# Performance work log

Hardware: AMD Instinct MI355X
Metric: run time of the kernel (lower is better)

## Reference

```python
import jax, jax.numpy as jnp
import numpy as np

EPS = 1e-12

def _l2n(x):
    # torch F.normalize(p=2, dim=0): x / max(||x||_2, eps)
    return x / jnp.maximum(jnp.linalg.norm(x), EPS)

def _gru_cell(x, h, Wi, Wh, bi, bh):
    # torch GRU cell math; Wi:(3H,Din), Wh:(3H,H)
    gi = Wi @ x + bi
    gh = Wh @ h + bh
    i_r, i_z, i_n = jnp.split(gi, 3)
    h_r, h_z, h_n = jnp.split(gh, 3)
    r = jax.nn.sigmoid(i_r + h_r)
    z = jax.nn.sigmoid(i_z + h_z)
    n = jnp.tanh(i_n + r * h_n)
    return (1.0 - z) * n + z * h

def setup_inputs() -> dict:
    key = jax.random.key(0)
    ks = jax.random.split(key, 20)
    m, n, T = 10, 10, 100
    H1, H2, HID = 1600, 400, 2000
    D_in, D_out = 2 * m + n, m * n
    f32 = jnp.float32
    inp = {
        'y': jax.random.normal(ks[0], (n, T), f32),
        'm1x_0': jax.random.normal(ks[1], (m,), f32),
        'F': jax.random.normal(ks[2], (m, m), f32) * 0.1,
        'Hm': jax.random.normal(ks[3], (n, m), f32) * 0.1,
        'h0': jax.random.normal(ks[4], (2, HID), f32),
        'W1': jax.random.normal(ks[5], (H1, D_in), f32) * 0.05,
        'b1': jax.random.normal(ks[6], (H1,), f32) * 0.05,
        'Wi0': jax.random.normal(ks[7], (3 * HID, H1), f32) * 0.02,
        'Wh0': jax.random.normal(ks[8], (3 * HID, HID), f32) * 0.02,
        'bi0': jax.random.normal(ks[9], (3 * HID,), f32) * 0.02,
        'bh0': jax.random.normal(ks[10], (3 * HID,), f32) * 0.02,
        'Wi1': jax.random.normal(ks[11], (3 * HID, HID), f32) * 0.02,
        'Wh1': jax.random.normal(ks[12], (3 * HID, HID), f32) * 0.02,
        'bi1': jax.random.normal(ks[13], (3 * HID,), f32) * 0.02,
        'bh1': jax.random.normal(ks[14], (3 * HID,), f32) * 0.02,
        'W2': jax.random.normal(ks[15], (H2, HID), f32) * 0.02,
        'b2': jax.random.normal(ks[16], (H2,), f32) * 0.02,
        'W3': jax.random.normal(ks[17], (D_out, H2), f32) * 0.01,
        'b3': jax.random.normal(ks[18], (D_out,), f32) * 0.01,
    }
    return inp

def reference(y, m1x_0, F, Hm, h0, W1, b1, Wi0, Wh0, bi0, bh0,
              Wi1, Wh1, bi1, bh1, W2, b2, W3, b3):
    n, T = y.shape
    m = m1x_0.shape[0]
    # first step uses obs_process_0 = h(f(m1x_0)) as y_previous surrogate
    y_prev0 = Hm @ (F @ m1x_0)
    carry0 = (m1x_0, jnp.zeros_like(m1x_0), m1x_0, y_prev0, h0[0], h0[1])

    def step(carry, yt):
        post, prev_post, prev_prior, y_prev, h1, h2 = carry
        prior = F @ post              # step_prior
        m1y = Hm @ prior
        f1 = _l2n(yt - y_prev)        # innovation diff feature
        f3 = _l2n(post - prev_post)   # posterior update feature
        f4 = _l2n(post - prev_prior)  # residual feature
        kin = jnp.concatenate([f1, f3, f4])  # (2m+n,)
        a = jax.nn.relu(W1 @ kin + b1)
        h1n = _gru_cell(a, h1, Wi0, Wh0, bi0, bh0)
        h2n = _gru_cell(h1n, h2, Wi1, Wh1, bi1, bh1)
        g = jax.nn.relu(W2 @ h2n + b2)
        KG = (W3 @ g + b3).reshape(m, n)
        dy = yt - m1y
        new_post = prior + KG @ dy
        return (new_post, post, prior, yt, h1n, h2n), new_post

    _, xs = jax.lax.scan(step, carry0, y.T)  # xs: (T, m)
    return xs.T  # (m, T)
```

## Files before the change

### kernel.cpp

```cpp
#include <hip/hip_runtime.h>
#include <math.h>

#define NB 256
#define NT 1024
#define NW 16
#define TT 100
#define MM 10
#define NN 10
#define HID 2000
#define H1 1600
#define H2 400
#define G3 6000
#define KP 2048
#define RPB 24

#define SCOPE_AGENT __HIP_MEMORY_SCOPE_AGENT

typedef _Float16 h2v __attribute__((ext_vector_type(2)));

__device__ __forceinline__ float sigf(float x) { return 1.f / (1.f + __expf(-x)); }
__device__ __forceinline__ float tanhfast(float x) { return 2.f / (1.f + __expf(-2.f * x)) - 1.f; }

__device__ __forceinline__ float ld_coh(const float* p) {
  return __hip_atomic_load(p, __ATOMIC_RELAXED, SCOPE_AGENT);
}
__device__ __forceinline__ void st_coh(float* p, float v) {
  __hip_atomic_store(p, v, __ATOMIC_RELAXED, SCOPE_AGENT);
}
__device__ __forceinline__ float2 ld_coh2(const float* p) {
  unsigned long long v = __hip_atomic_load((const unsigned long long*)p,
                                           __ATOMIC_RELAXED, SCOPE_AGENT);
  union { unsigned long long u; float2 f; } c; c.u = v; return c.f;
}
__device__ __forceinline__ void stage_coh(const float* __restrict__ src,
                                          float* __restrict__ dst, int n, int tid) {
  const int n2 = n >> 1;
  for (int j = tid; j < n2; j += NT) {
    float2 v = ld_coh2(src + 2 * j);
    dst[2 * j]     = v.x;
    dst[2 * j + 1] = v.y;
  }
}

__device__ __forceinline__ void gridbar(unsigned* flags, unsigned* release,
                                        unsigned ep, int tid, int blk) {
  __syncthreads();
  if (tid == 0)
    __hip_atomic_store(flags + blk * 16, ep, __ATOMIC_RELAXED, SCOPE_AGENT);
  if (blk == 0) {
    if (tid < NB) {
      while (__hip_atomic_load(flags + tid * 16, __ATOMIC_RELAXED, SCOPE_AGENT) < ep)
        __builtin_amdgcn_s_sleep(1);
    }
    __syncthreads();
    if (tid == 0)
      __hip_atomic_store(release, ep, __ATOMIC_RELAXED, SCOPE_AGENT);
  } else {
    if (tid == 0) {
      while (__hip_atomic_load(release, __ATOMIC_RELAXED, SCOPE_AGENT) < ep)
        __builtin_amdgcn_s_sleep(1);
    }
  }
  __syncthreads();
}

__device__ __forceinline__ void set_flag(unsigned* f, unsigned v, int tid) {
  __syncthreads();
  if (tid == 0) __hip_atomic_store(f, v, __ATOMIC_RELAXED, SCOPE_AGENT);
}
__device__ __forceinline__ void wait_flag(const unsigned* f, unsigned v, int tid) {
  if (tid == 0) {
    while (__hip_atomic_load(f, __ATOMIC_RELAXED, SCOPE_AGENT) < v)
      __builtin_amdgcn_s_sleep(1);
  }
  __syncthreads();
}

template<int K>
__device__ __forceinline__ float rowdotT(const float* __restrict__ row,
                                         const float* __restrict__ x, int ln) {
  constexpr int NFULL = K / 256;
  constexpr int REM   = K - NFULL * 256;
  const int base = ln * 4;
  float4 w[NFULL + (REM ? 1 : 0)];
  #pragma unroll
  for (int i = 0; i < NFULL; ++i)
    w[i] = *reinterpret_cast<const float4*>(row + base + i * 256);
  bool tail = false;
  if constexpr (REM != 0) {
    tail = (base + NFULL * 256 + 3 < K);
    if (tail) w[NFULL] = *reinterpret_cast<const float4*>(row + base + NFULL * 256);
  }
  float acc = 0.f;
  #pragma unroll
  for (int i = 0; i < NFULL; ++i) {
    const float4 xv = *reinterpret_cast<const float4*>(x + base + i * 256);
    acc = fmaf(w[i].x, xv.x, acc);
    acc = fmaf(w[i].y, xv.y, acc);
    acc = fmaf(w[i].z, xv.z, acc);
    acc = fmaf(w[i].w, xv.w, acc);
  }
  if constexpr (REM != 0) {
    if (tail) {
      const float4 xv = *reinterpret_cast<const float4*>(x + base + NFULL * 256);
      acc = fmaf(w[NFULL].x, xv.x, acc);
      acc = fmaf(w[NFULL].y, xv.y, acc);
      acc = fmaf(w[NFULL].z, xv.z, acc);
      acc = fmaf(w[NFULL].w, xv.w, acc);
    }
  }
  #pragma unroll
  for (int off = 32; off; off >>= 1) acc += __shfl_xor(acc, off, 64);
  return acc;
}

__device__ __forceinline__ void sweep24(const _Float16* __restrict__ W,
                                        const float* __restrict__ bias,
                                        int row0, int nrows,
                                        const _Float16* __restrict__ xh,
                                        float* __restrict__ outw,
                                        bool relu,
                                        int wv, int ln, int tid, float* red,
                                        float* __restrict__ gloc)
{
  const _Float16* wp = W + (size_t)row0 * KP + wv * 3072 + ln * 8;
  uint4 w[6];
  #pragma unroll
  for (int c = 0; c < 6; ++c)
    w[c] = *reinterpret_cast<const uint4*>(wp + c * 512);
  float a0 = 0.f, a1 = 0.f;
  const int first = (3 * wv) >> 1;
  #pragma unroll
  for (int c = 0; c < 6; ++c) {
    const int flat = wv * 3072 + c * 512;
    const int sel  = (flat >> 11) - first;
    const int col  = (flat & (KP - 1)) + ln * 8;
    const uint4 xv = *reinterpret_cast<const uint4*>(xh + col);
    union { uint4 u; h2v h[4]; } wu, xu;
    wu.u = w[c]; xu.u = xv;
    float acc = sel ? a1 : a0;
    #pragma unroll
    for (int q = 0; q < 4; ++q)
      acc = __builtin_amdgcn_fdot2(wu.h[q], xu.h[q], acc, false);
    if (sel) a1 = acc; else a0 = acc;
  }
  #pragma unroll
  for (int off = 32; off; off >>= 1) {
    a0 += __shfl_xor(a0, off, 64);
    a1 += __shfl_xor(a1, off, 64);
  }
  __syncthreads();
  if (ln == 0) { red[wv * 2] = a0; red[wv * 2 + 1] = a1; }
  __syncthreads();
  if (tid < nrows) {
    const int k = tid / 3, m = tid % 3;
    float v = (m == 0) ? red[4 * k]
            : (m == 1) ? red[4 * k + 1] + red[4 * k + 2]
                       : red[4 * k + 3];
    v += bias[row0 + tid];
    if (relu) v = fmaxf(v, 0.f);
    if (gloc) gloc[tid] = v;
    st_coh(outw + row0 + tid, v);
  }
}

__global__ __launch_bounds__(256)
void convh(const float* __restrict__ src, _Float16* __restrict__ dst,
           int rows, int K, int padrows) {
  const size_t total = (size_t)padrows * KP;
  for (size_t i = (size_t)blockIdx.x * blockDim.x + threadIdx.x; i < total;
       i += (size_t)gridDim.x * blockDim.x) {
    const int r = (int)(i >> 11), c = (int)(i & (KP - 1));
    float v = (r < rows && c < K) ? src[(size_t)r * K + c] : 0.f;
    dst[i] = (_Float16)v;
  }
}
__global__ __launch_bounds__(256)
void convw1(const float* __restrict__ src, _Float16* __restrict__ dst) {
  const int i = blockIdx.x * 256 + threadIdx.x;
  const int r = i >> 5, c = i & 31;
  float v = (r < H1 && c < 30) ? src[r * 30 + c] : 0.f;
  dst[i] = (_Float16)v;
}

__global__ __launch_bounds__(NT)
void knet_f16(const float* __restrict__ y, const float* __restrict__ m1x0,
              const float* __restrict__ F, const float* __restrict__ Hm,
              const float* __restrict__ h0,
              const float* __restrict__ W1, const float* __restrict__ b1,
              const float* __restrict__ Wi0, const float* __restrict__ Wh0,
              const float* __restrict__ bi0, const float* __restrict__ bh0,
              const float* __restrict__ Wi1, const float* __restrict__ Wh1,
              const float* __restrict__ bi1, const float* __restrict__ bh1,
              const float* __restrict__ W2, const float* __restrict__ b2,
              const float* __restrict__ W3, const float* __restrict__ b3,
              float* __restrict__ out, float* __restrict__ ws)
{
  const int blk = blockIdx.x, tid = threadIdx.x;
  const int wv = tid >> 6, ln = tid & 63;

  float* a_ws     = ws;
  float* gi0_ws   = ws + 1600;
  float* gh0_ws   = ws + 7600;
  float* gi1_ws   = ws + 13600;
  float* gh1b     = ws + 19600;
  float* g_ws     = ws + 31600;
  float* vpart_ws = ws + 32000;
  unsigned* flags   = (unsigned*)(ws + 33728);
  unsigned* release = flags + 256 * 16;
  unsigned* vflag   = release + 16;
  unsigned* aflag   = vflag + 17 * 16;

  const _Float16* whbase = (const _Float16*)((const char*)ws + 152576);
  const _Float16* Wi0h = whbase;
  const _Float16* Wh0h = whbase + (size_t)G3 * KP;
  const _Float16* Wi1h = whbase + (size_t)2 * G3 * KP;
  const _Float16* Wh1h = whbase + (size_t)3 * G3 * KP;
  const _Float16* W2h  = whbase + (size_t)4 * G3 * KP;
  const _Float16* W1h  = whbase + (size_t)4 * G3 * KP + (size_t)408 * KP;

  __shared__ __align__(16) _Float16 ah[KP];
  __shared__ __align__(16) _Float16 h1h[KP];
  __shared__ __align__(16) _Float16 h2h[KP];
  __shared__ __align__(16) float h1l[HID];
  __shared__ __align__(16) float h2l[HID];
  __shared__ __align__(16) float xs[1728];
  __shared__ __align__(16) _Float16 kin_h[32];
  __shared__ float red[32];
  __shared__ float gloc_s[RPB];
  __shared__ float post_s[MM], prevpost_s[MM], prevprior_s[MM], prior_s[MM];
  __shared__ float dy_s[NN], yprev_s[NN], tmp_s[MM];
  __shared__ float d1_s[NN], d3_s[MM], d4_s[MM];
  __shared__ float kin_s[32], nrm_s[3];
  __shared__ float v_s[MM * NN], np_s[MM];

  for (int j = tid; j < HID; j += NT) {
    float v1 = h0[j], v2 = h0[HID + j];
    h1l[j] = v1; h2l[j] = v2;
    h1h[j] = (_Float16)v1; h2h[j] = (_Float16)v2;
  }
  for (int j = HID + tid; j < KP; j += NT) { h1h[j] = (_Float16)0.f; h2h[j] = (_Float16)0.f; }
  for (int j = H1 + tid; j < KP; j += NT) ah[j] = (_Float16)0.f;
  __syncthreads();

  unsigned ep = 0;

  for (int t = 0; t < TT; ++t) {
    float* gh1w = gh1b + (t & 1) * G3;
    float* gh1r = gh1b + ((t + 1) & 1) * G3;

    if (blk == NB - 1) {
      if (t > 0) {
        if (tid < 17) {
          while (__hip_atomic_load(vflag + tid * 16, __ATOMIC_RELAXED, SCOPE_AGENT) < (unsigned)t)
            __builtin_amdgcn_s_sleep(1);
        }
        __syncthreads();
        stage_coh(vpart_ws, xs, 1700, tid);
        __syncthreads();
        if (tid < MM * NN) {
          float s = b3[tid];
          #pragma unroll
          for (int k = 0; k < 17; ++k) s += xs[k * 100 + tid];
          v_s[tid] = s;
        }
        __syncthreads();
        if (tid < MM) {
          float np = prior_s[tid];
          #pragma unroll
          for (int j = 0; j < NN; ++j) np = fmaf(v_s[tid * NN + j], dy_s[j], np);
          out[tid * TT + (t - 1)] = np;
          np_s[tid] = np;
        }
        __syncthreads();
        if (tid < MM) {
          prevpost_s[tid]  = post_s[tid];
          prevprior_s[tid] = prior_s[tid];
          post_s[tid]      = np_s[tid];
        }
        __syncthreads();
      } else {
        if (tid < MM) {
          post_s[tid]      = m1x0[tid];
          prevpost_s[tid]  = 0.f;
          prevprior_s[tid] = m1x0[tid];
          float tv = 0.f;
          for (int j = 0; j < MM; ++j) tv = fmaf(F[tid * MM + j], m1x0[j], tv);
          tmp_s[tid] = tv;
        }
        __syncthreads();
        if (tid < NN) {
          float yp = 0.f;
          for (int j = 0; j < MM; ++j) yp = fmaf(Hm[tid * MM + j], tmp_s[j], yp);
          yprev_s[tid] = yp;
        }
        __syncthreads();
      }
      if (tid < MM) {
        float pr = 0.f;
        for (int j = 0; j < MM; ++j) pr = fmaf(F[tid * MM + j], post_s[j], pr);
        prior_s[tid] = pr;
      }
      __syncthreads();
      if (tid < NN) {
        float my = 0.f;
        for (int j = 0; j < MM; ++j) my = fmaf(Hm[tid * MM + j], prior_s[j], my);
        float yt = y[tid * TT + t];
        dy_s[tid] = yt - my;
        d1_s[tid] = yt - ((t == 0) ? yprev_s[tid] : y[tid * TT + (t - 1)]);
        d3_s[tid] = post_s[tid] - prevpost_s[tid];
        d4_s[tid] = post_s[tid] - prevprior_s[tid];
      }
      __syncthreads();
      if (tid == 0) {
        float n1 = 0.f, n3 = 0.f, n4 = 0.f;
        for (int j = 0; j < NN; ++j) n1 += d1_s[j] * d1_s[j];
        for (int j = 0; j < MM; ++j) { n3 += d3_s[j] * d3_s[j]; n4 += d4_s[j] * d4_s[j]; }
        nrm_s[0] = fmaxf(sqrtf(n1), 1e-12f);
        nrm_s[1] = fmaxf(sqrtf(n3), 1e-12f);
        nrm_s[2] = fmaxf(sqrtf(n4), 1e-12f);
      }
      __syncthreads();
      if (tid < NN) kin_s[tid] = d1_s[tid] / nrm_s[0];
      if (tid < MM) {
        kin_s[NN + tid]      = d3_s[tid] / nrm_s[1];
        kin_s[NN + MM + tid] = d4_s[tid] / nrm_s[2];
      }
      __syncthreads();
      if (tid < 32) kin_h[tid] = (_Float16)((tid < 30) ? kin_s[tid] : 0.f);
      __syncthreads();
      if (tid < 800) {
        const _Float16* wp = W1h + (size_t)tid * 64;
        uint4 q[8];
        #pragma unroll
        for (int c = 0; c < 8; ++c)
          q[c] = *reinterpret_cast<const uint4*>(wp + c * 8);
        const uint4* kq = reinterpret_cast<const uint4*>(kin_h);
        union { uint4 u; h2v h[4]; } kk[4], qq;
        #pragma unroll
        for (int c = 0; c < 4; ++c) kk[c].u = kq[c];
        const int r0 = 2 * tid;
        float s0 = b1[r0], s1 = b1[r0 + 1];
        #pragma unroll
        for (int c = 0; c < 4; ++c) {
          qq.u = q[c];
          #pragma unroll
          for (int p = 0; p < 4; ++p)
            s0 = __builtin_amdgcn_fdot2(qq.h[p], kk[c].h[p], s0, false);
        }
        #pragma unroll
        for (int c = 0; c < 4; ++c) {
          qq.u = q[c + 4];
          #pragma unroll
          for (int p = 0; p < 4; ++p)
            s1 = __builtin_amdgcn_fdot2(qq.h[p], kk[c].h[p], s1, false);
        }
        st_coh(a_ws + r0,     fmaxf(s0, 0.f));
        st_coh(a_ws + r0 + 1, fmaxf(s1, 0.f));
      }
      set_flag(aflag, (unsigned)(t + 1), tid);
    } else {
      if (blk >= 17) {
        if (blk <= 249) {
          sweep24(Wh0h, bh0, RPB * (blk - 17), RPB, h1h, gh0_ws, false, wv, ln, tid, red, nullptr);
        } else {
          #pragma unroll
          for (int i = 0; i < 4; ++i) {
            const int task = 233 + (blk - 250) + 5 * i;
            if (task < 250)
              sweep24(Wh0h, bh0, RPB * task, RPB, h1h, gh0_ws, false, wv, ln, tid, red, nullptr);
          }
        }
      }
      if (t > 0) {
        for (int j = tid; j < HID / 2; j += NT) {
          float2 ir = ld_coh2(gi1_ws + 2 * j),            hr = ld_coh2(gh1r + 2 * j);
          float2 iz = ld_coh2(gi1_ws + HID + 2 * j),      hz = ld_coh2(gh1r + HID + 2 * j);
          float2 in_ = ld_coh2(gi1_ws + 2 * HID + 2 * j), hn = ld_coh2(gh1r + 2 * HID + 2 * j);
          float r0 = sigf(ir.x + hr.x), r1 = sigf(ir.y + hr.y);
          float z0 = sigf(iz.x + hz.x), z1 = sigf(iz.y + hz.y);
          float n0 = tanhfast(in_.x + r0 * hn.x), n1 = tanhfast(in_.y + r1 * hn.y);
          float o0 = (1.f - z0) * n0 + z0 * h2l[2 * j];
          float o1 = (1.f - z1) * n1 + z1 * h2l[2 * j + 1];
          h2l[2 * j] = o0; h2l[2 * j + 1] = o1;
          h2h[2 * j] = (_Float16)o0; h2h[2 * j + 1] = (_Float16)o1;
        }
        __syncthreads();
        if (blk < 17) {
          const int row0 = RPB * blk;
          const int nr = (H2 - row0 < RPB) ? (H2 - row0) : RPB;
          sweep24(W2h, b2, row0, nr, h2h, g_ws, true, wv, ln, tid, red, gloc_s);
          __syncthreads();
          if (tid < MM * NN) {
            float s = 0.f;
            const float* w3c = W3 + (size_t)tid * H2 + row0;
            for (int j = 0; j < nr; ++j) s = fmaf(w3c[j], gloc_s[j], s);
            st_coh(vpart_ws + blk * 100 + tid, s);
          }
          set_flag(vflag + blk * 16, (unsigned)t, tid);
        }
      }
      if (blk <= 249)
        sweep24(Wh1h, bh1, RPB * blk, RPB, h2h, gh1w, false, wv, ln, tid, red, nullptr);
      if (blk <= 249) {
        wait_flag(aflag, (unsigned)(t + 1), tid);
        const int n2 = H1 >> 1;
        for (int j = tid; j < n2; j += NT) {
          float2 v = ld_coh2(a_ws + 2 * j);
          ah[2 * j]     = (_Float16)v.x;
          ah[2 * j + 1] = (_Float16)v.y;
        }
        __syncthreads();
        sweep24(Wi0h, bi0, RPB * blk, RPB, ah, gi0_ws, false, wv, ln, tid, red, nullptr);
      }
    }
    ++ep; gridbar(flags, release, ep, tid, blk);

    if (blk != NB - 1) {
      for (int j = tid; j < HID / 2; j += NT) {
        float2 ir = ld_coh2(gi0_ws + 2 * j),            hr = ld_coh2(gh0_ws + 2 * j);
        float2 iz = ld_coh2(gi0_ws + HID + 2 * j),      hz = ld_coh2(gh0_ws + HID + 2 * j);
        float2 in_ = ld_coh2(gi0_ws + 2 * HID + 2 * j), hn = ld_coh2(gh0_ws + 2 * HID + 2 * j);
        float r0 = sigf(ir.x + hr.x), r1 = sigf(ir.y + hr.y);
        float z0 = sigf(iz.x + hz.x), z1 = sigf(iz.y + hz.y);
        float n0 = tanhfast(in_.x + r0 * hn.x), n1 = tanhfast(in_.y + r1 * hn.y);
        float o0 = (1.f - z0) * n0 + z0 * h1l[2 * j];
        float o1 = (1.f - z1) * n1 + z1 * h1l[2 * j + 1];
        h1l[2 * j] = o0; h1l[2 * j + 1] = o1;
        h1h[2 * j] = (_Float16)o0; h1h[2 * j + 1] = (_Float16)o1;
      }
      __syncthreads();
      if (blk <= 249)
        sweep24(Wi1h, bi1, RPB * blk, RPB, h1h, gi1_ws, false, wv, ln, tid, red, nullptr);
    }
    ++ep; gridbar(flags, release, ep, tid, blk);
  }

  if (blk < 17) {
    float* gh1r = gh1b + ((TT + 1) & 1) * G3;
    for (int j = tid; j < HID / 2; j += NT) {
      float2 ir = ld_coh2(gi1_ws + 2 * j),            hr = ld_coh2(gh1r + 2 * j);
      float2 iz = ld_coh2(gi1_ws + HID + 2 * j),      hz = ld_coh2(gh1r + HID + 2 * j);
      float2 in_ = ld_coh2(gi1_ws + 2 * HID + 2 * j), hn = ld_coh2(gh1r + 2 * HID + 2 * j);
      float r0 = sigf(ir.x + hr.x), r1 = sigf(ir.y + hr.y);
      float z0 = sigf(iz.x + hz.x), z1 = sigf(iz.y + hz.y);
      float n0 = tanhfast(in_.x + r0 * hn.x), n1 = tanhfast(in_.y + r1 * hn.y);
      float o0 = (1.f - z0) * n0 + z0 * h2l[2 * j];
      float o1 = (1.f - z1) * n1 + z1 * h2l[2 * j + 1];
      h2h[2 * j] = (_Float16)o0; h2h[2 * j + 1] = (_Float16)o1;
    }
    __syncthreads();
    const int row0 = RPB * blk;
    const int nr = (H2 - row0 < RPB) ? (H2 - row0) : RPB;
    sweep24(W2h, b2, row0, nr, h2h, g_ws, true, wv, ln, tid, red, gloc_s);
    __syncthreads();
    if (tid < MM * NN) {
      float s = 0.f;
      const float* w3c = W3 + (size_t)tid * H2 + row0;
      for (int j = 0; j < nr; ++j) s = fmaf(w3c[j], gloc_s[j], s);
      st_coh(vpart_ws + blk * 100 + tid, s);
    }
    set_flag(vflag + blk * 16, (unsigned)TT, tid);
  }
  if (blk == NB - 1) {
    if (tid < 17) {
      while (__hip_atomic_load(vflag + tid * 16, __ATOMIC_RELAXED, SCOPE_AGENT) < (unsigned)TT)
        __builtin_amdgcn_s_sleep(1);
    }
    __syncthreads();
    stage_coh(vpart_ws, xs, 1700, tid);
    __syncthreads();
    if (tid < MM * NN) {
      float s = b3[tid];
      #pragma unroll
      for (int k = 0; k < 17; ++k) s += xs[k * 100 + tid];
      v_s[tid] = s;
    }
    __syncthreads();
    if (tid < MM) {
      float np = prior_s[tid];
      #pragma unroll
      for (int j = 0; j < NN; ++j) np = fmaf(v_s[tid * NN + j], dy_s[j], np);
      out[tid * TT + (TT - 1)] = np;
    }
  }
}

__global__ __launch_bounds__(NT)
void knet_f32(const float* __restrict__ y, const float* __restrict__ m1x0,
              const float* __restrict__ F, const float* __restrict__ Hm,
              const float* __restrict__ h0,
              const float* __restrict__ W1, const float* __restrict__ b1,
              const float* __restrict__ Wi0, const float* __restrict__ Wh0,
              const float* __restrict__ bi0, const float* __restrict__ bh0,
              const float* __restrict__ Wi1, const float* __restrict__ Wh1,
              const float* __restrict__ bi1, const float* __restrict__ bh1,
              const float* __restrict__ W2, const float* __restrict__ b2,
              const float* __restrict__ W3, const float* __restrict__ b3,
              float* __restrict__ out, float* __restrict__ ws)
{
  const int blk = blockIdx.x, tid = threadIdx.x;
  const int wv = tid >> 6, ln = tid & 63;

  float* a_ws   = ws;
  float* gi0_ws = ws + 1600;
  float* gh0_ws = ws + 7600;
  float* gi1_ws = ws + 13600;
  float* gh1_ws = ws + 19600;
  float* g_ws   = ws + 25600;
  unsigned* flags   = (unsigned*)(ws + 26624);
  unsigned* release = flags + NB * 16;

  __shared__ __align__(16) float xs[1664];
  __shared__ __align__(16) float h1l[HID];
  __shared__ __align__(16) float h2l[HID];
  __shared__ float post_s[MM], prevpost_s[MM], prevprior_s[MM], prior_s[MM];
  __shared__ float dy_s[NN], yprev_s[NN], tmp_s[MM];
  __shared__ float d1_s[NN], d3_s[MM], d4_s[MM];
  __shared__ float kin_s[32], nrm_s[3];
  __shared__ float v_s[MM * NN], np_s[MM];

  for (int j = tid; j < HID; j += NT) { h1l[j] = h0[j]; h2l[j] = h0[HID + j]; }
  __syncthreads();

  unsigned ep = 0;

  for (int t = 0; t < TT; ++t) {
    if (blk == NB - 1) {
      if (t > 0) {
        stage_coh(g_ws, xs, H2, tid);
        __syncthreads();
        for (int r = wv; r < MM * NN; r += NW) {
          float acc = rowdotT<H2>(W3 + (size_t)r * H2, xs, ln);
          if (ln == 0) v_s[r] = acc + b3[r];
        }
        __syncthreads();
        if (tid < MM) {
          float np = prior_s[tid];
          #pragma unroll
          for (int j = 0; j < NN; ++j) np = fmaf(v_s[tid * NN + j], dy_s[j], np);
          out[tid * TT + (t - 1)] = np;
          np_s[tid] = np;
        }
        __syncthreads();
        if (tid < MM) {
          prevpost_s[tid]  = post_s[tid];
          prevprior_s[tid] = prior_s[tid];
          post_s[tid]      = np_s[tid];
        }
        __syncthreads();
      } else {
        if (tid < MM) {
          post_s[tid]      = m1x0[tid];
          prevpost_s[tid]  = 0.f;
          prevprior_s[tid] = m1x0[tid];
          float tv = 0.f;
          for (int j = 0; j < MM; ++j) tv = fmaf(F[tid * MM + j], m1x0[j], tv);
          tmp_s[tid] = tv;
        }
        __syncthreads();
        if (tid < NN) {
          float yp = 0.f;
          for (int j = 0; j < MM; ++j) yp = fmaf(Hm[tid * MM + j], tmp_s[j], yp);
          yprev_s[tid] = yp;
        }
        __syncthreads();
      }
      if (tid < MM) {
        float pr = 0.f;
        for (int j = 0; j < MM; ++j) pr = fmaf(F[tid * MM + j], post_s[j], pr);
        prior_s[tid] = pr;
      }
      __syncthreads();
      if (tid < NN) {
        float my = 0.f;
        for (int j = 0; j < MM; ++j) my = fmaf(Hm[tid * MM + j], prior_s[j], my);
        float yt = y[tid * TT + t];
        dy_s[tid] = yt - my;
        d1_s[tid] = yt - ((t == 0) ? yprev_s[tid] : y[tid * TT + (t - 1)]);
        d3_s[tid] = post_s[tid] - prevpost_s[tid];
        d4_s[tid] = post_s[tid] - prevprior_s[tid];
      }
      __syncthreads();
      if (tid == 0) {
        float n1 = 0.f, n3 = 0.f, n4 = 0.f;
        for (int j = 0; j < NN; ++j) n1 += d1_s[j] * d1_s[j];
        for (int j = 0; j < MM; ++j) { n3 += d3_s[j] * d3_s[j]; n4 += d4_s[j] * d4_s[j]; }
        nrm_s[0] = fmaxf(sqrtf(n1), 1e-12f);
        nrm_s[1] = fmaxf(sqrtf(n3), 1e-12f);
        nrm_s[2] = fmaxf(sqrtf(n4), 1e-12f);
      }
      __syncthreads();
      if (tid < NN) kin_s[tid] = d1_s[tid] / nrm_s[0];
      if (tid < MM) {
        kin_s[NN + tid]      = d3_s[tid] / nrm_s[1];
        kin_s[NN + MM + tid] = d4_s[tid] / nrm_s[2];
      }
      __syncthreads();
      for (int r = tid; r < H1; r += NT) {
        float acc = b1[r];
        const float* row = W1 + (size_t)r * 30;
        #pragma unroll
        for (int k = 0; k < 30; ++k) acc = fmaf(row[k], kin_s[k], acc);
        st_coh(a_ws + r, fmaxf(acc, 0.f));
      }
    } else {
      const int gw = blk * NW + wv;
      for (int r = gw; r < G3; r += (NB - 1) * NW) {
        float acc = rowdotT<HID>(Wh1 + (size_t)r * HID, h2l, ln);
        if (ln == 0) st_coh(gh1_ws + r, acc + bh1[r]);
      }
      if (t == 0) {
        for (int r = gw; r < G3; r += (NB - 1) * NW) {
          float acc = rowdotT<HID>(Wh0 + (size_t)r * HID, h1l, ln);
          if (ln == 0) st_coh(gh0_ws + r, acc + bh0[r]);
        }
      }
    }
    ++ep; gridbar(flags, release, ep, tid, blk);

    stage_coh(a_ws, xs, H1, tid);
    __syncthreads();
    {
      const int gw = blk * NW + wv;
      for (int r = gw; r < G3; r += NB * NW) {
        float acc = rowdotT<H1>(Wi0 + (size_t)r * H1, xs, ln);
        if (ln == 0) st_coh(gi0_ws + r, acc + bi0[r]);
      }
    }
    ++ep; gridbar(flags, release, ep, tid, blk);

    {
      for (int j = tid; j < HID / 2; j += NT) {
        float2 ir = ld_coh2(gi0_ws + 2 * j),            hr = ld_coh2(gh0_ws + 2 * j);
        float2 iz = ld_coh2(gi0_ws + HID + 2 * j),      hz = ld_coh2(gh0_ws + HID + 2 * j);
        float2 in_ = ld_coh2(gi0_ws + 2 * HID + 2 * j), hn = ld_coh2(gh0_ws + 2 * HID + 2 * j);
        float r0 = sigf(ir.x + hr.x), r1 = sigf(ir.y + hr.y);
        float z0 = sigf(iz.x + hz.x), z1 = sigf(iz.y + hz.y);
        float n0 = tanhfast(in_.x + r0 * hn.x), n1 = tanhfast(in_.y + r1 * hn.y);
        h1l[2 * j]     = (1.f - z0) * n0 + z0 * h1l[2 * j];
        h1l[2 * j + 1] = (1.f - z1) * n1 + z1 * h1l[2 * j + 1];
      }
      __syncthreads();
      const int gw = blk * NW + wv;
      for (int r = gw; r < G3; r += NB * NW) {
        float acc = rowdotT<HID>(Wi1 + (size_t)r * HID, h1l, ln);
        if (ln == 0) st_coh(gi1_ws + r, acc + bi1[r]);
      }
    }
    ++ep; gridbar(flags, release, ep, tid, blk);

    {
      for (int j = tid; j < HID / 2; j += NT) {
        float2 ir = ld_coh2(gi1_ws + 2 * j),            hr = ld_coh2(gh1_ws + 2 * j);
        float2 iz = ld_coh2(gi1_ws + HID + 2 * j),      hz = ld_coh2(gh1_ws + HID + 2 * j);
        float2 in_ = ld_coh2(gi1_ws + 2 * HID + 2 * j), hn = ld_coh2(gh1_ws + 2 * HID + 2 * j);
        float r0 = sigf(ir.x + hr.x), r1 = sigf(ir.y + hr.y);
        float z0 = sigf(iz.x + hz.x), z1 = sigf(iz.y + hz.y);
        float n0 = tanhfast(in_.x + r0 * hn.x), n1 = tanhfast(in_.y + r1 * hn.y);
        h2l[2 * j]     = (1.f - z0) * n0 + z0 * h2l[2 * j];
        h2l[2 * j + 1] = (1.f - z1) * n1 + z1 * h2l[2 * j + 1];
      }
      __syncthreads();
      const int gw = blk * NW + wv;
      for (int r = gw; r < H2 + G3; r += NB * NW) {
        if (r < H2) {
          float acc = rowdotT<HID>(W2 + (size_t)r * HID, h2l, ln);
          if (ln == 0) st_coh(g_ws + r, fmaxf(acc + b2[r], 0.f));
        } else {
          const int rr = r - H2;
          float acc = rowdotT<HID>(Wh0 + (size_t)rr * HID, h1l, ln);
          if (ln == 0) st_coh(gh0_ws + rr, acc + bh0[rr]);
        }
      }
    }
    ++ep; gridbar(flags, release, ep, tid, blk);
  }

  if (blk == NB - 1) {
    stage_coh(g_ws, xs, H2, tid);
    __syncthreads();
    for (int r = wv; r < MM * NN; r += NW) {
      float acc = rowdotT<H2>(W3 + (size_t)r * H2, xs, ln);
      if (ln == 0) v_s[r] = acc + b3[r];
    }
    __syncthreads();
    if (tid < MM) {
      float np = prior_s[tid];
      #pragma unroll
      for (int j = 0; j < NN; ++j) np = fmaf(v_s[tid * NN + j], dy_s[j], np);
      out[tid * TT + (TT - 1)] = np;
    }
  }
}

extern "C" void kernel_launch(void* const* d_in, const int* in_sizes, int n_in,
                              void* d_out, int out_size, void* d_ws, size_t ws_size,
                              hipStream_t stream) {
  const float* y    = (const float*)d_in[0];
  const float* m1x0 = (const float*)d_in[1];
  const float* F    = (const float*)d_in[2];
  const float* Hm   = (const float*)d_in[3];
  const float* h0   = (const float*)d_in[4];
  const float* W1   = (const float*)d_in[5];
  const float* b1   = (const float*)d_in[6];
  const float* Wi0  = (const float*)d_in[7];
  const float* Wh0  = (const float*)d_in[8];
  const float* bi0  = (const float*)d_in[9];
  const float* bh0  = (const float*)d_in[10];
  const float* Wi1  = (const float*)d_in[11];
  const float* Wh1  = (const float*)d_in[12];
  const float* bi1  = (const float*)d_in[13];
  const float* bh1  = (const float*)d_in[14];
  const float* W2   = (const float*)d_in[15];
  const float* b2   = (const float*)d_in[16];
  const float* W3   = (const float*)d_in[17];
  const float* b3   = (const float*)d_in[18];
  float* out = (float*)d_out;
  float* ws  = (float*)d_ws;

  const size_t WBASE = 152576;
  const size_t NEED = WBASE +
      ((size_t)4 * G3 * KP + (size_t)408 * KP + (size_t)65536) * 2;

  void* args[] = { &y, &m1x0, &F, &Hm, &h0, &W1, &b1, &Wi0, &Wh0, &bi0, &bh0,
                   &Wi1, &Wh1, &bi1, &bh1, &W2, &b2, &W3, &b3, &out, &ws };

  if (ws_size >= NEED) {
    hipMemsetAsync((char*)d_ws + 33728 * sizeof(float), 0, 275 * 64, stream);
    _Float16* wh = (_Float16*)((char*)d_ws + WBASE);
    convh<<<2048, 256, 0, stream>>>(Wi0, wh,                         G3, H1,  G3);
    convh<<<2048, 256, 0, stream>>>(Wh0, wh + (size_t)G3 * KP,       G3, HID, G3);
    convh<<<2048, 256, 0, stream>>>(Wi1, wh + (size_t)2 * G3 * KP,   G3, HID, G3);
    convh<<<2048, 256, 0, stream>>>(Wh1, wh + (size_t)3 * G3 * KP,   G3, HID, G3);
    convh<<<2048, 256, 0, stream>>>(W2,  wh + (size_t)4 * G3 * KP,   H2, HID, 408);
    convw1<<<256, 256, 0, stream>>>(W1,  wh + (size_t)4 * G3 * KP + (size_t)408 * KP);
    hipLaunchCooperativeKernel((const void*)knet_f16, dim3(NB), dim3(NT),
                               args, 0, stream);
  } else {
    hipMemsetAsync((char*)d_ws + 26624 * sizeof(float), 0, NB * 64 + 64, stream);
    hipLaunchCooperativeKernel((const void*)knet_f32, dim3(NB), dim3(NT),
                               args, 0, stream);
  }
}
```

Measured before the change: 3.733 ms.

## Double persistent grid to 512 blocks and exchange GRU gates as packed fp16

Result: slower. 4.931 ms (+32.1%).

```diff
diff --git a/kernel.cpp b/kernel.cpp
--- a/kernel.cpp
+++ b/kernel.cpp
@@ -2,6 +2,7 @@
 #include <math.h>
 
 #define NB 256
+#define NBK 512
 #define NT 1024
 #define NW 16
 #define TT 100
@@ -21,9 +22,6 @@
 __device__ __forceinline__ float sigf(float x) { return 1.f / (1.f + __expf(-x)); }
 __device__ __forceinline__ float tanhfast(float x) { return 2.f / (1.f + __expf(-2.f * x)) - 1.f; }
 
-__device__ __forceinline__ float ld_coh(const float* p) {
-  return __hip_atomic_load(p, __ATOMIC_RELAXED, SCOPE_AGENT);
-}
 __device__ __forceinline__ void st_coh(float* p, float v) {
   __hip_atomic_store(p, v, __ATOMIC_RELAXED, SCOPE_AGENT);
 }
@@ -31,6 +29,12 @@
   unsigned long long v = __hip_atomic_load((const unsigned long long*)p,
                                            __ATOMIC_RELAXED, SCOPE_AGENT);
   union { unsigned long long u; float2 f; } c; c.u = v; return c.f;
+}
+__device__ __forceinline__ unsigned ld_coh_u32(const unsigned* p) {
+  return __hip_atomic_load(p, __ATOMIC_RELAXED, SCOPE_AGENT);
+}
+__device__ __forceinline__ void st_coh_u32(unsigned* p, unsigned v) {
+  __hip_atomic_store(p, v, __ATOMIC_RELAXED, SCOPE_AGENT);
 }
 __device__ __forceinline__ void stage_coh(const float* __restrict__ src,
                                           float* __restrict__ dst, int n, int tid) {
@@ -42,13 +46,23 @@
   }
 }
 
+__device__ __forceinline__ unsigned pack2(float a, float b) {
+  union { unsigned u; h2v h; } c;
+  c.h[0] = (_Float16)a; c.h[1] = (_Float16)b;
+  return c.u;
+}
+__device__ __forceinline__ float2 upk(unsigned u) {
+  union { unsigned u; h2v h; } c; c.u = u;
+  float2 r; r.x = (float)c.h[0]; r.y = (float)c.h[1]; return r;
+}
+
 __device__ __forceinline__ void gridbar(unsigned* flags, unsigned* release,
-                                        unsigned ep, int tid, int blk) {
+                                        unsigned ep, int tid, int blk, int nblk) {
   __syncthreads();
   if (tid == 0)
     __hip_atomic_store(flags + blk * 16, ep, __ATOMIC_RELAXED, SCOPE_AGENT);
   if (blk == 0) {
-    if (tid < NB) {
+    if (tid < nblk) {
       while (__hip_atomic_load(flags + tid * 16, __ATOMIC_RELAXED, SCOPE_AGENT) < ep)
         __builtin_amdgcn_s_sleep(1);
     }
@@ -118,7 +132,7 @@
                                         const float* __restrict__ bias,
                                         int row0, int nrows,
                                         const _Float16* __restrict__ xh,
-                                        float* __restrict__ outw,
+                                        unsigned* __restrict__ outp,
                                         bool relu,
                                         int wv, int ln, int tid, float* red,
                                         float* __restrict__ gloc)
@@ -159,9 +173,30 @@
                        : red[4 * k + 3];
     v += bias[row0 + tid];
     if (relu) v = fmaxf(v, 0.f);
-    if (gloc) gloc[tid] = v;
-    st_coh(outw + row0 + tid, v);
-  }
+    gloc[tid] = v;
+  }
+  __syncthreads();
+  if (outp && tid < (nrows >> 1))
+    st_coh_u32(outp + (row0 >> 1) + tid, pack2(gloc[2 * tid], gloc[2 * tid + 1]));
+}
+
+__device__ __forceinline__ void combine_gru(const unsigned* __restrict__ gip,
+                                            const unsigned* __restrict__ ghp,
+                                            float* __restrict__ hl,
+                                            _Float16* __restrict__ hh, int tid) {
+  for (int j = tid; j < HID / 2; j += NT) {
+    float2 ir = upk(ld_coh_u32(gip + j)),        hr = upk(ld_coh_u32(ghp + j));
+    float2 iz = upk(ld_coh_u32(gip + 1000 + j)), hz = upk(ld_coh_u32(ghp + 1000 + j));
+    float2 in_ = upk(ld_coh_u32(gip + 2000 + j)), hn = upk(ld_coh_u32(ghp + 2000 + j));
+    float r0 = sigf(ir.x + hr.x), r1 = sigf(ir.y + hr.y);
+    float z0 = sigf(iz.x + hz.x), z1 = sigf(iz.y + hz.y);
+    float n0 = tanhfast(in_.x + r0 * hn.x), n1 = tanhfast(in_.y + r1 * hn.y);
+    float o0 = (1.f - z0) * n0 + z0 * hl[2 * j];
+    float o1 = (1.f - z1) * n1 + z1 * hl[2 * j + 1];
+    hl[2 * j] = o0; hl[2 * j + 1] = o1;
+    hh[2 * j] = (_Float16)o0; hh[2 * j + 1] = (_Float16)o1;
+  }
+  __syncthreads();
 }
 
 __global__ __launch_bounds__(256)
@@ -183,7 +218,7 @@
   dst[i] = (_Float16)v;
 }
 
-__global__ __launch_bounds__(NT)
+__global__ __launch_bounds__(NT, 8)
 void knet_f16(const float* __restrict__ y, const float* __restrict__ m1x0,
               const float* __restrict__ F, const float* __restrict__ Hm,
               const float* __restrict__ h0,
@@ -199,19 +234,18 @@
   const int blk = blockIdx.x, tid = threadIdx.x;
   const int wv = tid >> 6, ln = tid & 63;
 
-  float* a_ws     = ws;
-  float* gi0_ws   = ws + 1600;
-  float* gh0_ws   = ws + 7600;
-  float* gi1_ws   = ws + 13600;
-  float* gh1b     = ws + 19600;
-  float* g_ws     = ws + 31600;
-  float* vpart_ws = ws + 32000;
-  unsigned* flags   = (unsigned*)(ws + 33728);
-  unsigned* release = flags + 256 * 16;
+  unsigned* gi0p = (unsigned*)ws;
+  unsigned* gh0p = gi0p + 3000;
+  unsigned* gi1p = gi0p + 6000;
+  unsigned* gh1p = gi0p + 9000;
+  float* vpart_ws  = ws + 15000;
+  unsigned* kinpack = (unsigned*)(ws + 16704);
+  unsigned* flags   = (unsigned*)(ws + 16720);
+  unsigned* release = flags + NBK * 16;
   unsigned* vflag   = release + 16;
-  unsigned* aflag   = vflag + 17 * 16;
-
-  const _Float16* whbase = (const _Float16*)((const char*)ws + 152576);
+  unsigned* kflag   = vflag + 17 * 16;
+
+  const _Float16* whbase = (const _Float16*)((const char*)ws + 131072);
   const _Float16* Wi0h = whbase;
   const _Float16* Wh0h = whbase + (size_t)G3 * KP;
   const _Float16* Wi1h = whbase + (size_t)2 * G3 * KP;
@@ -243,13 +277,15 @@
   for (int j = H1 + tid; j < KP; j += NT) ah[j] = (_Float16)0.f;
   __syncthreads();
 
+  const bool isSerial = (blk == NBK - 1);
+
   unsigned ep = 0;
 
   for (int t = 0; t < TT; ++t) {
-    float* gh1w = gh1b + (t & 1) * G3;
-    float* gh1r = gh1b + ((t + 1) & 1) * G3;
-
-    if (blk == NB - 1) {
+    unsigned* gh1wp = gh1p + (t & 1) * 3000;
+    const unsigned* gh1rp = gh1p + ((t + 1) & 1) * 3000;
+
+    if (isSerial) {
       if (t > 0) {
         if (tid < 17) {
           while (__hip_atomic_load(vflag + tid * 16, __ATOMIC_RELAXED, SCOPE_AGENT) < (unsigned)t)
@@ -329,6 +365,13 @@
       __syncthreads();
       if (tid < 32) kin_h[tid] = (_Float16)((tid < 30) ? kin_s[tid] : 0.f);
       __syncthreads();
+      if (tid < 16) st_coh_u32(kinpack + tid, ((const unsigned*)kin_h)[tid]);
+      set_flag(kflag, (unsigned)(t + 1), tid);
+    } else if (blk < 250) {
+      sweep24(Wh0h, bh0, RPB * blk, RPB, h1h, gh0p, false, wv, ln, tid, red, gloc_s);
+      wait_flag(kflag, (unsigned)(t + 1), tid);
+      if (tid < 16) ((unsigned*)kin_h)[tid] = ld_coh_u32(kinpack + tid);
+      __syncthreads();
       if (tid < 800) {
         const _Float16* wp = W1h + (size_t)tid * 64;
         uint4 q[8];
@@ -336,133 +379,87 @@
         for (int c = 0; c < 8; ++c)
           q[c] = *reinterpret_cast<const uint4*>(wp + c * 8);
         const uint4* kq = reinterpret_cast<const uint4*>(kin_h);
-        union { uint4 u; h2v h[4]; } kk[4], qq;
+        union U { uint4 u; h2v h[4]; };
+        U kk[4];
         #pragma unroll
         for (int c = 0; c < 4; ++c) kk[c].u = kq[c];
         const int r0 = 2 * tid;
         float s0 = b1[r0], s1 = b1[r0 + 1];
         #pragma unroll
         for (int c = 0; c < 4; ++c) {
-          qq.u = q[c];
+          U qq; qq.u = q[c];
           #pragma unroll
           for (int p = 0; p < 4; ++p)
             s0 = __builtin_amdgcn_fdot2(qq.h[p], kk[c].h[p], s0, false);
         }
         #pragma unroll
         for (int c = 0; c < 4; ++c) {
-          qq.u = q[c + 4];
+          U qq; qq.u = q[c + 4];
           #pragma unroll
           for (int p = 0; p < 4; ++p)
             s1 = __builtin_amdgcn_fdot2(qq.h[p], kk[c].h[p], s1, false);
         }
-        st_coh(a_ws + r0,     fmaxf(s0, 0.f));
-        st_coh(a_ws + r0 + 1, fmaxf(s1, 0.f));
-      }
-      set_flag(aflag, (unsigned)(t + 1), tid);
+        ah[r0]     = (_Float16)fmaxf(s0, 0.f);
+        ah[r0 + 1] = (_Float16)fmaxf(s1, 0.f);
+      }
+      __syncthreads();
+      sweep24(Wi0h, bi0, RPB * blk, RPB, ah, gi0p, false, wv, ln, tid, red, gloc_s);
     } else {
-      if (blk >= 17) {
-        if (blk <= 249) {
-          sweep24(Wh0h, bh0, RPB * (blk - 17), RPB, h1h, gh0_ws, false, wv, ln, tid, red, nullptr);
-        } else {
-          #pragma unroll
-          for (int i = 0; i < 4; ++i) {
-            const int task = 233 + (blk - 250) + 5 * i;
-            if (task < 250)
-              sweep24(Wh0h, bh0, RPB * task, RPB, h1h, gh0_ws, false, wv, ln, tid, red, nullptr);
+      if (t > 0) combine_gru(gi1p, gh1rp, h2l, h2h, tid);
+      if (blk < 500) {
+        sweep24(Wh1h, bh1, RPB * (blk - 250), RPB, h2h, gh1wp, false, wv, ln, tid, red, gloc_s);
+      } else if (t > 0) {
+        #pragma unroll
+        for (int rep = 0; rep < 2; ++rep) {
+          const int task = (rep == 0) ? (blk - 500) : (blk - 489);
+          if (task < 17) {
+            const int row0 = RPB * task;
+            const int nr = (H2 - row0 < RPB) ? (H2 - row0) : RPB;
+            sweep24(W2h, b2, row0, nr, h2h, nullptr, true, wv, ln, tid, red, gloc_s);
+            __syncthreads();
+            if (tid < MM * NN) {
+              float s = 0.f;
+              const float* w3c = W3 + (size_t)tid * H2 + row0;
+              for (int j = 0; j < nr; ++j) s = fmaf(w3c[j], gloc_s[j], s);
+              st_coh(vpart_ws + task * 100 + tid, s);
+            }
+            set_flag(vflag + task * 16, (unsigned)t, tid);
           }
         }
       }
-      if (t > 0) {
-        for (int j = tid; j < HID / 2; j += NT) {
-          float2 ir = ld_coh2(gi1_ws + 2 * j),            hr = ld_coh2(gh1r + 2 * j);
-          float2 iz = ld_coh2(gi1_ws + HID + 2 * j),      hz = ld_coh2(gh1r + HID + 2 * j);
-          float2 in_ = ld_coh2(gi1_ws + 2 * HID + 2 * j), hn = ld_coh2(gh1r + 2 * HID + 2 * j);
-          float r0 = sigf(ir.x + hr.x), r1 = sigf(ir.y + hr.y);
-          float z0 = sigf(iz.x + hz.x), z1 = sigf(iz.y + hz.y);
-          float n0 = tanhfast(in_.x + r0 * hn.x), n1 = tanhfast(in_.y + r1 * hn.y);
-          float o0 = (1.f - z0) * n0 + z0 * h2l[2 * j];
-          float o1 = (1.f - z1) * n1 + z1 * h2l[2 * j + 1];
-          h2l[2 * j] = o0; h2l[2 * j + 1] = o1;
-          h2h[2 * j] = (_Float16)o0; h2h[2 * j + 1] = (_Float16)o1;
-        }
-        __syncthreads();
-        if (blk < 17) {
-          const int row0 = RPB * blk;
-          const int nr = (H2 - row0 < RPB) ? (H2 - row0) : RPB;
-          sweep24(W2h, b2, row0, nr, h2h, g_ws, true, wv, ln, tid, red, gloc_s);
-          __syncthreads();
-          if (tid < MM * NN) {
-            float s = 0.f;
-            const float* w3c = W3 + (size_t)tid * H2 + row0;
-            for (int j = 0; j < nr; ++j) s = fmaf(w3c[j], gloc_s[j], s);
-            st_coh(vpart_ws + blk * 100 + tid, s);
-          }
-          set_flag(vflag + blk * 16, (unsigned)t, tid);
-        }
-      }
-      if (blk <= 249)
-        sweep24(Wh1h, bh1, RPB * blk, RPB, h2h, gh1w, false, wv, ln, tid, red, nullptr);
-      if (blk <= 249) {
-        wait_flag(aflag, (unsigned)(t + 1), tid);
-        const int n2 = H1 >> 1;
-        for (int j = tid; j < n2; j += NT) {
-          float2 v = ld_coh2(a_ws + 2 * j);
-          ah[2 * j]     = (_Float16)v.x;
-          ah[2 * j + 1] = (_Float16)v.y;
-        }
-        __syncthreads();
-        sweep24(Wi0h, bi0, RPB * blk, RPB, ah, gi0_ws, false, wv, ln, tid, red, nullptr);
-      }
-    }
-    ++ep; gridbar(flags, release, ep, tid, blk);
-
-    if (blk != NB - 1) {
-      for (int j = tid; j < HID / 2; j += NT) {
-        float2 ir = ld_coh2(gi0_ws + 2 * j),            hr = ld_coh2(gh0_ws + 2 * j);
-        float2 iz = ld_coh2(gi0_ws + HID + 2 * j),      hz = ld_coh2(gh0_ws + HID + 2 * j);
-        float2 in_ = ld_coh2(gi0_ws + 2 * HID + 2 * j), hn = ld_coh2(gh0_ws + 2 * HID + 2 * j);
-        float r0 = sigf(ir.x + hr.x), r1 = sigf(ir.y + hr.y);
-        float z0 = sigf(iz.x + hz.x), z1 = sigf(iz.y + hz.y);
-        float n0 = tanhfast(in_.x + r0 * hn.x), n1 = tanhfast(in_.y + r1 * hn.y);
-        float o0 = (1.f - z0) * n0 + z0 * h1l[2 * j];
-        float o1 = (1.f - z1) * n1 + z1 * h1l[2 * j + 1];
-        h1l[2 * j] = o0; h1l[2 * j + 1] = o1;
-        h1h[2 * j] = (_Float16)o0; h1h[2 * j + 1] = (_Float16)o1;
-      }
-      __syncthreads();
-      if (blk <= 249)
-        sweep24(Wi1h, bi1, RPB * blk, RPB, h1h, gi1_ws, false, wv, ln, tid, red, nullptr);
-    }
-    ++ep; gridbar(flags, release, ep, tid, blk);
-  }
-
-  if (blk < 17) {
-    float* gh1r = gh1b + ((TT + 1) & 1) * G3;
-    for (int j = tid; j < HID / 2; j += NT) {
-      float2 ir = ld_coh2(gi1_ws + 2 * j),            hr = ld_coh2(gh1r + 2 * j);
-      float2 iz = ld_coh2(gi1_ws + HID + 2 * j),      hz = ld_coh2(gh1r + HID + 2 * j);
-      float2 in_ = ld_coh2(gi1_ws + 2 * HID + 2 * j), hn = ld_coh2(gh1r + 2 * HID + 2 * j);
-      float r0 = sigf(ir.x + hr.x), r1 = sigf(ir.y + hr.y);
-      float z0 = sigf(iz.x + hz.x), z1 = sigf(iz.y + hz.y);
-      float n0 = tanhfast(in_.x + r0 * hn.x), n1 = tanhfast(in_.y + r1 * hn.y);
-      float o0 = (1.f - z0) * n0 + z0 * h2l[2 * j];
-      float o1 = (1.f - z1) * n1 + z1 * h2l[2 * j + 1];
-      h2h[2 * j] = (_Float16)o0; h2h[2 * j + 1] = (_Float16)o1;
-    }
-    __syncthreads();
-    const int row0 = RPB * blk;
-    const int nr = (H2 - row0 < RPB) ? (H2 - row0) : RPB;
-    sweep24(W2h, b2, row0, nr, h2h, g_ws, true, wv, ln, tid, red, gloc_s);
-    __syncthreads();
-    if (tid < MM * NN) {
-      float s = 0.f;
-      const float* w3c = W3 + (size_t)tid * H2 + row0;
-      for (int j = 0; j < nr; ++j) s = fmaf(w3c[j], gloc_s[j], s);
-      st_coh(vpart_ws + blk * 100 + tid, s);
-    }
-    set_flag(vflag + blk * 16, (unsigned)TT, tid);
-  }
-  if (blk == NB - 1) {
+    }
+    ++ep; gridbar(flags, release, ep, tid, blk, NBK);
+
+    if (!isSerial && blk < 500) {
+      combine_gru(gi0p, gh0p, h1l, h1h, tid);
+      if (blk >= 250)
+        sweep24(Wi1h, bi1, RPB * (blk - 250), RPB, h1h, gi1p, false, wv, ln, tid, red, gloc_s);
+    }
+    ++ep; gridbar(flags, release, ep, tid, blk, NBK);
+  }
+
+  if (blk >= 500 && blk < NBK - 1) {
+    const unsigned* gh1fp = gh1p + ((TT + 1) & 1) * 3000;
+    combine_gru(gi1p, gh1fp, h2l, h2h, tid);
+    #pragma unroll
+    for (int rep = 0; rep < 2; ++rep) {
+      const int task = (rep == 0) ? (blk - 500) : (blk - 489);
+      if (task < 17) {
+        const int row0 = RPB * task;
+        const int nr = (H2 - row0 < RPB) ? (H2 - row0) : RPB;
+        sweep24(W2h, b2, row0, nr, h2h, nullptr, true, wv, ln, tid, red, gloc_s);
+        __syncthreads();
+        if (tid < MM * NN) {
+          float s = 0.f;
+          const float* w3c = W3 + (size_t)tid * H2 + row0;
+          for (int j = 0; j < nr; ++j) s = fmaf(w3c[j], gloc_s[j], s);
+          st_coh(vpart_ws + task * 100 + tid, s);
+        }
+        set_flag(vflag + task * 16, (unsigned)TT, tid);
+      }
+    }
+  }
+  if (isSerial) {
     if (tid < 17) {
       while (__hip_atomic_load(vflag + tid * 16, __ATOMIC_RELAXED, SCOPE_AGENT) < (unsigned)TT)
         __builtin_amdgcn_s_sleep(1);
@@ -617,7 +614,7 @@
         }
       }
     }
-    ++ep; gridbar(flags, release, ep, tid, blk);
+    ++ep; gridbar(flags, release, ep, tid, blk, NB);
 
     stage_coh(a_ws, xs, H1, tid);
     __syncthreads();
@@ -628,7 +625,7 @@
         if (ln == 0) st_coh(gi0_ws + r, acc + bi0[r]);
       }
     }
-    ++ep; gridbar(flags, release, ep, tid, blk);
+    ++ep; gridbar(flags, release, ep, tid, blk, NB);
 
     {
       for (int j = tid; j < HID / 2; j += NT) {
@@ -648,7 +645,7 @@
         if (ln == 0) st_coh(gi1_ws + r, acc + bi1[r]);
       }
     }
-    ++ep; gridbar(flags, release, ep, tid, blk);
+    ++ep; gridbar(flags, release, ep, tid, blk, NB);
 
     {
       for (int j = tid; j < HID / 2; j += NT) {
@@ -674,7 +671,7 @@
         }
       }
     }
-    ++ep; gridbar(flags, release, ep, tid, blk);
+    ++ep; gridbar(flags, release, ep, tid, blk, NB);
   }
 
   if (blk == NB - 1) {
@@ -719,15 +716,18 @@
   float* out = (float*)d_out;
   float* ws  = (float*)d_ws;
 
-  const size_t WBASE = 152576;
+  const size_t WBASE = 131072;
   const size_t NEED = WBASE +
       ((size_t)4 * G3 * KP + (size_t)408 * KP + (size_t)65536) * 2;
 
   void* args[] = { &y, &m1x0, &F, &Hm, &h0, &W1, &b1, &Wi0, &Wh0, &bi0, &bh0,
                    &Wi1, &Wh1, &bi1, &bh1, &W2, &b2, &W3, &b3, &out, &ws };
 
-  if (ws_size >= NEED) {
-    hipMemsetAsync((char*)d_ws + 33728 * sizeof(float), 0, 275 * 64, stream);
+  int occ = 0;
+  hipOccupancyMaxActiveBlocksPerMultiprocessor(&occ, (const void*)knet_f16, NT, 0);
+
+  if (ws_size >= NEED && occ >= 2) {
+    hipMemsetAsync((char*)d_ws + 16720 * 4, 0, (25216 - 16720) * 4, stream);
     _Float16* wh = (_Float16*)((char*)d_ws + WBASE);
     convh<<<2048, 256, 0, stream>>>(Wi0, wh,                         G3, H1,  G3);
     convh<<<2048, 256, 0, stream>>>(Wh0, wh + (size_t)G3 * KP,       G3, HID, G3);
@@ -735,7 +735,7 @@
     convh<<<2048, 256, 0, stream>>>(Wh1, wh + (size_t)3 * G3 * KP,   G3, HID, G3);
     convh<<<2048, 256, 0, stream>>>(W2,  wh + (size_t)4 * G3 * KP,   H2, HID, 408);
     convw1<<<256, 256, 0, stream>>>(W1,  wh + (size_t)4 * G3 * KP + (size_t)408 * KP);
-    hipLaunchCooperativeKernel((const void*)knet_f16, dim3(NB), dim3(NT),
+    hipLaunchCooperativeKernel((const void*)knet_f16, dim3(NBK), dim3(NT),
                                args, 0, stream);
   } else {
     hipMemsetAsync((char*)d_ws + 26624 * sizeof(float), 0, NB * 64 + 64, stream);
```
